# Kernel optimization log

Measured on AMD Instinct MI355X. Metric: run time of the kernel, lower is better.

## Reference

```python
import jax, jax.numpy as jnp
import numpy as np

M = 128  # template / canvas size (hardcoded in the module)


def _pair_indices(nodes_per_image):
    # Static (host-side) ragged pair construction, mirroring the Python loop
    # in the torch forward. Returns compressed index arrays for valid pairs.
    npi = np.asarray(nodes_per_image)
    idx_a, idx_b, batch, valid = [], [], [], []
    off = 0
    for b, n in enumerate(npi.tolist()):
        a = np.repeat(np.arange(n), n) + off   # repeat_interleave
        c = np.tile(np.arange(n), n) + off     # .repeat(n, 1)
        idx_a.append(a); idx_b.append(c)
        batch.append(np.full(n * n, b))
        if n > 1:
            v = np.triu(np.ones((n, n)), 1).astype(bool).reshape(-1)
        else:
            v = np.zeros((n * n,), bool)
        valid.append(v)
        off += n
    return (np.concatenate(idx_a), np.concatenate(idx_b),
            np.concatenate(batch), np.concatenate(valid))


def _grid_sample_bilinear(img, gx, gy):
    # img [O, M, M]; gx, gy [O, H, W] in [-1, 1]; align_corners=True, zero padding
    ix = (gx + 1.0) * 0.5 * (M - 1)
    iy = (gy + 1.0) * 0.5 * (M - 1)
    x0 = jnp.floor(ix); y0 = jnp.floor(iy)
    wx = ix - x0; wy = iy - y0
    out = jnp.zeros_like(gx)
    corners = ((0, 0, (1 - wy) * (1 - wx)), (0, 1, (1 - wy) * wx),
               (1, 0, wy * (1 - wx)), (1, 1, wy * wx))
    for dy, dx, w in corners:
        xi = x0 + dx; yi = y0 + dy
        inb = (xi >= 0) & (xi <= M - 1) & (yi >= 0) & (yi <= M - 1)
        xc = jnp.clip(xi, 0, M - 1).astype(jnp.int32)
        yc = jnp.clip(yi, 0, M - 1).astype(jnp.int32)
        v = jax.vmap(lambda m, yy, xx: m[yy, xx])(img, yc, xc)
        out = out + w * jnp.where(inb, v, 0.0)
    return out


def masks_to_layout(vecs, boxes, masks, obj_to_img, num_images, H):
    # sg2im-style: warp each mask into its box, scale by vec, scatter-add per image
    x0 = boxes[:, 0][:, None, None]; y0 = boxes[:, 1][:, None, None]
    x1 = boxes[:, 2][:, None, None]; y1 = boxes[:, 3][:, None, None]
    X = jnp.linspace(0.0, 1.0, H)[None, None, :]   # [1,1,W]
    Y = jnp.linspace(0.0, 1.0, H)[None, :, None]   # [1,H,1]
    gx = ((X - x0) / (x1 - x0)) * 2.0 - 1.0        # [O,1,W]
    gy = ((Y - y0) / (y1 - y0)) * 2.0 - 1.0        # [O,H,1]
    O = boxes.shape[0]
    gx = jnp.broadcast_to(gx, (O, H, H))
    gy = jnp.broadcast_to(gy, (O, H, H))
    sampled = _grid_sample_bilinear(masks, gx, gy)           # [O,H,W]
    sampled = sampled * vecs[:, 0][:, None, None]            # D = 1 channel
    out = jax.ops.segment_sum(sampled, obj_to_img, num_segments=num_images)
    return out[:, None]  # [B,1,H,W] (segment_sum already zero-pads empty images)


def _forward(nodes, adj_mat, nodes_per_image):
    ii = jnp.arange(M)
    # eye(128) max-pooled with k=11, s=1, p=5 -> band of half-width 10
    line_template = (jnp.abs(ii[:, None] - ii[None, :]) <= 10).astype(jnp.float32)
    idx_a, idx_b, batch_ids, valid = _pair_indices(nodes_per_image)
    sel = np.nonzero(valid)[0]
    idx_a = idx_a[sel]; idx_b = idx_b[sel]
    obj_to_img = jnp.asarray(batch_ids[sel], dtype=jnp.int32)
    boxes = jnp.concatenate([nodes[idx_a], nodes[idx_b]], axis=1)  # [O,4]
    vecs = adj_mat[sel]                                            # [O,1]
    B = int(np.asarray(nodes_per_image).shape[0])
    dual_slope = (jnp.abs((boxes[:, 3] - boxes[:, 1]) / (jnp.abs(boxes[:, 2] - boxes[:, 0]) + 1e-6))
                  + jnp.abs((boxes[:, 2] - boxes[:, 0]) / (jnp.abs(boxes[:, 3] - boxes[:, 1]) + 1e-6)))
    t = jnp.clip(2.0 * jax.nn.sigmoid(0.03 * (dual_slope - 2.0)) - 1.0, 0.0, 1.0)
    t = t[:, None, None]
    masks = (1.0 - t) * line_template[None, :, :] + t  # rect_template == ones
    img = masks_to_layout(vecs, boxes, masks, obj_to_img, B, M)
    return jnp.clip(img, 0.0, 1.0)


def setup_inputs() -> dict:
    key = jax.random.key(0)
    k1, k2 = jax.random.split(key)
    B, n = 24, 16
    nodes = jax.random.uniform(k1, (B * n, 2), dtype=jnp.float32)       # [384,2] in [0,1]
    adj_mat = jax.random.uniform(k2, (B * n * n, 1), dtype=jnp.float32)  # [6144,1]
    nodes_per_image = np.full((B,), n, dtype=np.int64)  # static ragged sizes
    return {"nodes": nodes, "adj_mat": adj_mat, "nodes_per_image": nodes_per_image}


def reference(nodes, adj_mat, nodes_per_image):
    return _forward(nodes, adj_mat, nodes_per_image)
```

## Files before the change

### kernel.cpp

```cpp
#include <hip/hip_runtime.h>

#define MM    128
#define NN    16
#define NPAIR 120
#define NIMG  24
#define ROWS_PER_BLK 2
#define STRIPS 64
#define NWIN   4
#define CAP    121

__global__ __launch_bounds__(256) void g2i_kernel(
    const float* __restrict__ nodes,
    const float* __restrict__ adj,
    float* __restrict__ out)
{
    __shared__ float2 s_ab [NWIN][CAP];
    __shared__ float4 s_row[NWIN][CAP * ROWS_PER_BLK];
    __shared__ int    s_cnt[NWIN];

    const int img   = blockIdx.x >> 6;
    const int strip = (((blockIdx.x & 63) * 21) + img * 7) & 63;
    const int r0    = strip * ROWS_PER_BLK;
    const int tid   = threadIdx.x;

    if (tid < NWIN) s_cnt[tid] = 0;
    __syncthreads();

    if (tid < NPAIR) {
        int k = tid, i = 0;
        while (k >= (NN - 1 - i)) { k -= (NN - 1 - i); ++i; }
        const int j = i + 1 + k;
        const float x0 = nodes[(img * NN + i) * 2 + 0];
        const float y0 = nodes[(img * NN + i) * 2 + 1];
        const float x1 = nodes[(img * NN + j) * 2 + 0];
        const float y1 = nodes[(img * NN + j) * 2 + 1];
        const float dx = x1 - x0, dy = y1 - y0;

        const float ya  = 127.0f * y0 - dy;
        const float yb  = 127.0f * y0 + 128.0f * dy;
        const float ylo = fminf(ya, yb) - 0.5f;
        const float yhi = fmaxf(ya, yb) + 0.5f;

        if (yhi >= (float)r0 && ylo <= (float)(r0 + ROWS_PER_BLK - 1)) {
            const float ds = fabsf(dy) / (fabsf(dx) + 1e-6f)
                           + fabsf(dx) / (fabsf(dy) + 1e-6f);
            float t = 2.0f / (1.0f + expf(-0.03f * (ds - 2.0f))) - 1.0f;
            t = fminf(fmaxf(t, 0.0f), 1.0f);
            const float vec = adj[img * NN * NN + i * NN + j];
            const float p = vec * t;
            const float q = vec * (1.0f - t);

            const float cay = 1.0f / dy;
            const float cby = -127.0f * y0 / dy;
            float4 rd[ROWS_PER_BLK];
            #pragma unroll
            for (int r = 0; r < ROWS_PER_BLK; ++r) {
                const float iy  = (float)(r0 + r) * cay + cby;
                const float y0f = floorf(iy);
                const float wy  = iy - y0f;
                const float ey0 = (y0f >=  0.0f && y0f <= 127.0f) ? (1.0f - wy) : 0.0f;
                const float ey1 = (y0f >= -1.0f && y0f <= 126.0f) ? wy          : 0.0f;
                rd[r] = make_float4(q * ey0, q * ey1, p * (ey0 + ey1), y0f);
            }

            const float2 ab = make_float2(1.0f / dx, -127.0f * x0 / dx);
            const float xa  = 127.0f * x0 - dx;
            const float xb  = 127.0f * x0 + 128.0f * dx;
            const float xlo = fminf(xa, xb) - 0.5f;
            const float xhi = fmaxf(xa, xb) + 0.5f;

            #pragma unroll
            for (int w = 0; w < NWIN; ++w) {
                const float wl = (float)(w * 32) - 0.5f;
                const float wh = (float)(w * 32) + 31.5f;
                if (xhi >= wl && xlo <= wh) {
                    const int slot = atomicAdd(&s_cnt[w], 1);
                    s_ab [w][slot] = ab;
                    s_row[w][slot * ROWS_PER_BLK + 0] = rd[0];
                    s_row[w][slot * ROWS_PER_BLK + 1] = rd[1];
                }
            }
        }
    }
    __syncthreads();

    const int w    = tid >> 6;
    const int lane = tid & 63;
    const int px   = (w << 5) + (lane & 31);
    const int row  = lane >> 5;
    const int py   = r0 + row;
    const float fx = (float)px;
    const int  cnt = s_cnt[w];

    float acc = 0.0f;
    float2 ab_n = s_ab[w][0];
    float4 ry_n = s_row[w][row];

    for (int s = 0; s < cnt; ++s) {
        const float2 ab = ab_n;
        const float4 ry = ry_n;
        ab_n = s_ab[w][s + 1];
        ry_n = s_row[w][(s + 1) * ROWS_PER_BLK + row];

        const float ix  = fmaf(fx, ab.x, ab.y);
        const float x0f = floorf(ix);
        const float wx  = ix - x0f;
        const float ex0 = (x0f >=  0.0f && x0f <= 127.0f) ? (1.0f - wx) : 0.0f;
        const float ex1 = (x0f >= -1.0f && x0f <= 126.0f) ? wx          : 0.0f;

        const float df  = ry.w - x0f;
        const float l00 = (fabsf(df)        <= 10.0f) ? 1.0f : 0.0f;
        const float l01 = (fabsf(df - 1.0f) <= 10.0f) ? 1.0f : 0.0f;
        const float l10 = (fabsf(df + 1.0f) <= 10.0f) ? 1.0f : 0.0f;

        acc = fmaf(ry.z, ex0 + ex1, acc);
        acc = fmaf(ry.x, fmaf(ex0, l00, ex1 * l01), acc);
        acc = fmaf(ry.y, fmaf(ex0, l10, ex1 * l00), acc);
    }

    acc = fminf(fmaxf(acc, 0.0f), 1.0f);
    out[(size_t)img * (MM * MM) + py * MM + px] = acc;
}

extern "C" void kernel_launch(void* const* d_in, const int* in_sizes, int n_in,
                              void* d_out, int out_size, void* d_ws, size_t ws_size,
                              hipStream_t stream) {
    const float* nodes = (const float*)d_in[0];
    const float* adj   = (const float*)d_in[1];
    float* out = (float*)d_out;
    g2i_kernel<<<dim3(NIMG * STRIPS), dim3(256), 0, stream>>>(nodes, adj, out);
}
```

Measured before the change: 69.15 us.

## Reformulate per-pixel bilinear line weights as clamped tent functions precomputed per pair

Rewrites the inner per-pixel loop so that the floor-based bilinear weights and band masks are replaced by clamped linear ramps (med3) computed from per-pair, per-row constants precomputed in shared memory. Setup math is also switched to fast reciprocal and exp intrinsics, and node loads are vectorized to float2. The aim is fewer ALU ops per pair per pixel in the hot loop. The cost is more shared memory per slot and possible small numerical differences from approximate reciprocals.

```diff
diff --git a/kernel.cpp b/kernel.cpp
--- a/kernel.cpp
+++ b/kernel.cpp
@@ -4,23 +4,23 @@
 #define NN    16
 #define NPAIR 120
 #define NIMG  24
-#define ROWS_PER_BLK 2
+#define ROWS  2
 #define STRIPS 64
-#define NWIN   4
-#define CAP    121
+#define NWIN  4
+#define CAP   121
 
 __global__ __launch_bounds__(256) void g2i_kernel(
     const float* __restrict__ nodes,
     const float* __restrict__ adj,
     float* __restrict__ out)
 {
-    __shared__ float2 s_ab [NWIN][CAP];
-    __shared__ float4 s_row[NWIN][CAP * ROWS_PER_BLK];
+    __shared__ float4 s_AB[NWIN][CAP * 4];
+    __shared__ float  s_c [NWIN][CAP];
     __shared__ int    s_cnt[NWIN];
 
     const int img   = blockIdx.x >> 6;
     const int strip = (((blockIdx.x & 63) * 21) + img * 7) & 63;
-    const int r0    = strip * ROWS_PER_BLK;
+    const int r0    = strip * ROWS;
     const int tid   = threadIdx.x;
 
     if (tid < NWIN) s_cnt[tid] = 0;
@@ -30,42 +30,51 @@
         int k = tid, i = 0;
         while (k >= (NN - 1 - i)) { k -= (NN - 1 - i); ++i; }
         const int j = i + 1 + k;
-        const float x0 = nodes[(img * NN + i) * 2 + 0];
-        const float y0 = nodes[(img * NN + i) * 2 + 1];
-        const float x1 = nodes[(img * NN + j) * 2 + 0];
-        const float y1 = nodes[(img * NN + j) * 2 + 1];
+        const float2 na = ((const float2*)nodes)[img * NN + i];
+        const float2 nb = ((const float2*)nodes)[img * NN + j];
+        const float x0 = na.x, y0 = na.y, x1 = nb.x, y1 = nb.y;
         const float dx = x1 - x0, dy = y1 - y0;
 
         const float ya  = 127.0f * y0 - dy;
-        const float yb  = 127.0f * y0 + 128.0f * dy;
+        const float yb  = ya + 129.0f * dy;
         const float ylo = fminf(ya, yb) - 0.5f;
         const float yhi = fmaxf(ya, yb) + 0.5f;
 
-        if (yhi >= (float)r0 && ylo <= (float)(r0 + ROWS_PER_BLK - 1)) {
-            const float ds = fabsf(dy) / (fabsf(dx) + 1e-6f)
-                           + fabsf(dx) / (fabsf(dy) + 1e-6f);
-            float t = 2.0f / (1.0f + expf(-0.03f * (ds - 2.0f))) - 1.0f;
+        if (yhi >= (float)r0 && ylo <= (float)(r0 + ROWS - 1)) {
+            const float adx = fabsf(dx), ady = fabsf(dy);
+            const float ds  = ady * __builtin_amdgcn_rcpf(adx + 1e-6f)
+                            + adx * __builtin_amdgcn_rcpf(ady + 1e-6f);
+            const float e = __expf(-0.03f * (ds - 2.0f));
+            float t = fmaf(2.0f, __builtin_amdgcn_rcpf(1.0f + e), -1.0f);
             t = fminf(fmaxf(t, 0.0f), 1.0f);
             const float vec = adj[img * NN * NN + i * NN + j];
             const float p = vec * t;
             const float q = vec * (1.0f - t);
 
-            const float cay = 1.0f / dy;
-            const float cby = -127.0f * y0 / dy;
-            float4 rd[ROWS_PER_BLK];
+            const float cax = __builtin_amdgcn_rcpf(dx);
+            const float cbx = -127.0f * x0 * cax;
+            const float cay = __builtin_amdgcn_rcpf(dy);
+            const float cby = -127.0f * y0 * cay;
+
+            float4 Ar[ROWS], Br[ROWS];
             #pragma unroll
-            for (int r = 0; r < ROWS_PER_BLK; ++r) {
+            for (int r = 0; r < ROWS; ++r) {
                 const float iy  = (float)(r0 + r) * cay + cby;
                 const float y0f = floorf(iy);
                 const float wy  = iy - y0f;
                 const float ey0 = (y0f >=  0.0f && y0f <= 127.0f) ? (1.0f - wy) : 0.0f;
                 const float ey1 = (y0f >= -1.0f && y0f <= 126.0f) ? wy          : 0.0f;
-                rd[r] = make_float4(q * ey0, q * ey1, p * (ey0 + ey1), y0f);
+                const float A0 = fmaxf(0.0f,   y0f - 10.0f);
+                const float B0 = fminf(127.0f, y0f + 10.0f);
+                const float A1 = fmaxf(0.0f,   y0f -  9.0f);
+                const float B1 = fminf(127.0f, y0f + 11.0f);
+                Ar[r] = make_float4(-A0 + 1.0f, B0 - A0 + 2.0f,
+                                    -A1 + 1.0f, B1 - A1 + 2.0f);
+                Br[r] = make_float4(p * (ey0 + ey1), q * ey0, q * ey1, A0);
             }
 
-            const float2 ab = make_float2(1.0f / dx, -127.0f * x0 / dx);
             const float xa  = 127.0f * x0 - dx;
-            const float xb  = 127.0f * x0 + 128.0f * dx;
+            const float xb  = xa + 129.0f * dx;
             const float xlo = fminf(xa, xb) - 0.5f;
             const float xhi = fmaxf(xa, xb) + 0.5f;
 
@@ -75,9 +84,14 @@
                 const float wh = (float)(w * 32) + 31.5f;
                 if (xhi >= wl && xlo <= wh) {
                     const int slot = atomicAdd(&s_cnt[w], 1);
-                    s_ab [w][slot] = ab;
-                    s_row[w][slot * ROWS_PER_BLK + 0] = rd[0];
-                    s_row[w][slot * ROWS_PER_BLK + 1] = rd[1];
+                    const float base = fmaf((float)(w * 32), cax, cbx);
+                    #pragma unroll
+                    for (int r = 0; r < ROWS; ++r) {
+                        s_AB[w][slot * 4 + r * 2 + 0] =
+                            make_float4(base + Ar[r].x, Ar[r].y, base + Ar[r].z, Ar[r].w);
+                        s_AB[w][slot * 4 + r * 2 + 1] = Br[r];
+                    }
+                    s_c[w][slot] = cax;
                 }
             }
         }
@@ -86,36 +100,40 @@
 
     const int w    = tid >> 6;
     const int lane = tid & 63;
-    const int px   = (w << 5) + (lane & 31);
+    const int lx   = lane & 31;
     const int row  = lane >> 5;
+    const int px   = (w << 5) + lx;
     const int py   = r0 + row;
-    const float fx = (float)px;
-    const int  cnt = s_cnt[w];
+    const float fl = (float)lx;
+    const int cnt  = s_cnt[w];
+
+    const float4* __restrict__ AB = &s_AB[w][row * 2];
+    const float*  __restrict__ C  = &s_c[w][0];
 
     float acc = 0.0f;
-    float2 ab_n = s_ab[w][0];
-    float4 ry_n = s_row[w][row];
+    float4 a_n = AB[0];
+    float4 b_n = AB[1];
+    float  c_n = C[0];
 
     for (int s = 0; s < cnt; ++s) {
-        const float2 ab = ab_n;
-        const float4 ry = ry_n;
-        ab_n = s_ab[w][s + 1];
-        ry_n = s_row[w][(s + 1) * ROWS_PER_BLK + row];
+        const float4 a = a_n;
+        const float4 b = b_n;
+        const float ca = c_n;
+        a_n = AB[(s + 1) * 4 + 0];
+        b_n = AB[(s + 1) * 4 + 1];
+        c_n = C[s + 1];
 
-        const float ix  = fmaf(fx, ab.x, ab.y);
-        const float x0f = floorf(ix);
-        const float wx  = ix - x0f;
-        const float ex0 = (x0f >=  0.0f && x0f <= 127.0f) ? (1.0f - wx) : 0.0f;
-        const float ex1 = (x0f >= -1.0f && x0f <= 126.0f) ? wx          : 0.0f;
-
-        const float df  = ry.w - x0f;
-        const float l00 = (fabsf(df)        <= 10.0f) ? 1.0f : 0.0f;
-        const float l01 = (fabsf(df - 1.0f) <= 10.0f) ? 1.0f : 0.0f;
-        const float l10 = (fabsf(df + 1.0f) <= 10.0f) ? 1.0f : 0.0f;
-
-        acc = fmaf(ry.z, ex0 + ex1, acc);
-        acc = fmaf(ry.x, fmaf(ex0, l00, ex1 * l01), acc);
-        acc = fmaf(ry.y, fmaf(ex0, l10, ex1 * l00), acc);
+        const float z0 = fmaf(fl, ca, a.x);
+        const float s0 = a.y - z0;
+        const float z1 = fmaf(fl, ca, a.z);
+        const float s1 = a.w - z1;
+        const float zs = z0 + b.w;
+        const float t0 = __builtin_amdgcn_fmed3f(fminf(z0, s0), 0.0f, 1.0f);
+        const float t1 = __builtin_amdgcn_fmed3f(fminf(z1, s1), 0.0f, 1.0f);
+        const float ts = __builtin_amdgcn_fmed3f(fminf(zs, 129.0f - zs), 0.0f, 1.0f);
+        acc = fmaf(b.x, ts, acc);
+        acc = fmaf(b.y, t0, acc);
+        acc = fmaf(b.z, t1, acc);
     }
 
     acc = fminf(fmaxf(acc, 0.0f), 1.0f);
```

Measured after the change: 65.33 us. 5.5% less time.
